# Kernel tuning notes

Measured on AMD Instinct MI355X. Metric: run time of the kernel, lower is better.

The kernel has to match this reference:

```python
import jax, jax.numpy as jnp
import numpy as np

N_OBJS = 100          # max detections / scatter buffer size
TOP_K = 100           # top_k_n peaks per channel
KP_THRES = 0.3        # score threshold before NMS
NMS_IOU = 0.5
RESIZE_H, RESIZE_W = 1536.0, 1536.0   # resize_shape (== heatmap HxW here)
H, W = 1536, 1536


def _peak_hms(hms):
    # 3x3 stride-1 SAME max pool; keep only local maxima (Base.apply_max_pool)
    hmax = jax.lax.reduce_window(hms, -jnp.inf, jax.lax.max, (1, 3, 3, 1), (1, 1, 1, 1), 'SAME')
    return jnp.where(hms == hmax, hms, 0.0)


def _top_k_loc(hms, k):
    # per-channel top-k peak coordinates -> [b, c, k, 2] (y, x) int32
    b, h, w, c = hms.shape
    flat = jnp.transpose(hms, (0, 3, 1, 2)).reshape(b, c, h * w)
    _, idx = jax.lax.top_k(flat, k)
    return jnp.stack([idx // w, idx % w], axis=-1).astype(jnp.int32)


def _iou_matrix(boxes):
    # boxes [N,4] = (y1,x1,y2,x2)
    y1, x1, y2, x2 = boxes[:, 0], boxes[:, 1], boxes[:, 2], boxes[:, 3]
    area = jnp.maximum(y2 - y1, 0.0) * jnp.maximum(x2 - x1, 0.0)
    iy1 = jnp.maximum(y1[:, None], y1[None, :]); ix1 = jnp.maximum(x1[:, None], x1[None, :])
    iy2 = jnp.minimum(y2[:, None], y2[None, :]); ix2 = jnp.minimum(x2[:, None], x2[None, :])
    inter = jnp.maximum(iy2 - iy1, 0.0) * jnp.maximum(ix2 - ix1, 0.0)
    union = area[:, None] + area[None, :] - inter
    return inter / jnp.maximum(union, 1e-8)


def _nms_single(boxes, scores):
    # greedy single-class NMS, fixed-size (combined_non_max_suppression equivalent,
    # clip_boxes=False, score_threshold=-inf); padded slots are zeros like TF.
    order = jnp.argsort(-scores)
    boxes, scores = boxes[order], scores[order]
    n = boxes.shape[0]
    iou = _iou_matrix(boxes)
    idxs = jnp.arange(n)

    def step(suppressed, inp):
        i, iou_row = inp
        keep_i = ~suppressed[i]
        return suppressed | (keep_i & (iou_row > NMS_IOU) & (idxs > i)), keep_i

    _, keep = jax.lax.scan(step, jnp.zeros(n, bool), (idxs, iou))
    perm = jnp.argsort(jnp.where(keep, 0, 1))  # stable: compact kept to front, score order preserved
    keep_s = keep[perm]
    out_boxes = jnp.where(keep_s[:, None], boxes[perm], 0.0)
    out_scores = jnp.where(keep_s, scores[perm], 0.0)
    return out_boxes, out_scores, jnp.zeros(n, jnp.float32)


def _forward(obj_heat_map, offset_map, size_maps, origin_shapes):
    resize_shape = jnp.array([RESIZE_H, RESIZE_W], jnp.float32)
    ratio = origin_shapes / resize_shape                      # [b,2]
    hms = _peak_hms(obj_heat_map)                             # [b,H,W,2]
    b = hms.shape[0]
    coors = _top_k_loc(hms, TOP_K)                            # [b,2,K,2]
    b_coors, b_lnmks = coors[:, :1], coors[:, 1:]             # obj / nose coords
    bidx = jnp.arange(b)[:, None, None]

    # nose landmark: scores at nose-channel peaks, masked mean of coords (int mean like TF)
    nose_scores = hms[bidx, b_lnmks[..., 0], b_lnmks[..., 1], 1]     # [b,1,K]
    nose_mask = nose_scores > 0.5
    cnt = jnp.maximum(jnp.sum(nose_mask), 1)
    lnmk_mean = jnp.sum(jnp.where(nose_mask[..., None], b_lnmks, 0), axis=(0, 1, 2)) // cnt
    b_lnmks_m = lnmk_mean.reshape(b, 1, 2)                    # requires b == 1 (as in original)
    b_nose_scores = jnp.where(nose_mask, nose_scores, -1.0).reshape(b, -1)

    # boxes from sizes at object peaks
    size_vals = size_maps[bidx, b_coors[..., 0], b_coors[..., 1]]    # [b,1,K,2]
    obj_scores = hms[bidx, b_coors[..., 0], b_coors[..., 1], 0]      # [b,1,K]
    centers = b_coors.astype(jnp.float32)
    tls = jnp.maximum(centers - size_vals / 2.0, 0.0)
    brs = jnp.minimum(centers + size_vals / 2.0, resize_shape - 1.0)
    bboxes = jnp.concatenate([tls, brs], axis=-1) * jnp.tile(ratio, (1, 2))[:, None, None, :]
    bboxes, scores = bboxes[:, 0], obj_scores[:, 0]           # [b,K,4], [b,K]

    # scatter masked candidates into -1-initialized buffer (tensor_scatter_nd_update equivalent)
    mask = scores > KP_THRES
    cand = jnp.where(mask[..., None], jnp.concatenate([bboxes, scores[..., None]], -1), -1.0)
    cand = jnp.pad(cand, ((0, 0), (0, N_OBJS - TOP_K), (0, 0)), constant_values=-1.0)  # [b,N_OBJS,5]

    nb, ns, nc = jax.vmap(_nms_single)(cand[..., :4], cand[..., 4])
    box_results = jnp.where(nb == -1.0, jnp.inf, nb)
    box_results = jnp.where(box_results == 0.0, jnp.inf, box_results)  # (x - 1 == -1)
    b_bboxes = jnp.concatenate([box_results, ns[..., None], nc[..., None]], axis=-1)  # [b,N_OBJS,6]

    # offset vectors at the mean nose landmark (gather 8ch -> [b,n,4,2])
    bidx2 = jnp.arange(b)[:, None]
    off = offset_map[bidx2, b_lnmks_m[..., 0], b_lnmks_m[..., 1]].reshape(b, 1, 4, 2)
    lf = b_lnmks_m.astype(jnp.float32)
    b_ENM = (lf[:, :, None, :] - off) * ratio[:, None, None, :]
    b_lnmks_out = lf * ratio[:, None, :]
    return b_bboxes, b_lnmks_out, b_ENM, b_nose_scores


def setup_inputs() -> dict:
    key = jax.random.key(0)
    k1, k2, k3 = jax.random.split(key, 3)
    obj_heat_map = jax.random.uniform(k1, (1, H, W, 2), jnp.float32)
    offset_map = jax.random.normal(k2, (1, H, W, 8), jnp.float32) * 8.0
    size_maps = jax.random.uniform(k3, (1, H, W, 2), jnp.float32) * 128.0
    origin_shapes = jnp.array([[1080.0, 1920.0]], jnp.float32)
    return {"obj_heat_map": obj_heat_map, "offset_map": offset_map,
            "size_maps": size_maps, "origin_shapes": origin_shapes}


def reference(obj_heat_map, offset_map, size_maps, origin_shapes):
    return _forward(obj_heat_map, offset_map, size_maps, origin_shapes)
```

## Files before the change

kernel.cpp:

```cpp
#include <hip/hip_runtime.h>
#include <cstdint>

#define IW 1536
#define IH 1536
#define TOPK 100
#define CAPP 327680
#define CAPB 128
#define CAPM 16384
#define BF_INF16 0x7F7Fu

typedef unsigned u32; typedef unsigned long long u64; typedef unsigned short u16;

#define OH1   0
#define OCNT  512
#define OSEL  516
#define OPK   520
#define OPV   (OPK + 2*CAPP)
#define OMID  (OPV + CAPP)

__device__ __forceinline__ u32 enc16(u32 b){ b &= 0xFFFFu; return (b & 0x8000u) ? ((~b)&0xFFFFu) : (b|0x8000u); }
__device__ __forceinline__ u32 dec16(u32 e){ return (e & 0x8000u) ? (e^0x8000u) : ((~e)&0xFFFFu); }
__device__ __forceinline__ float up16(u32 b){ return __uint_as_float((b&0xFFFFu)<<16); }
__device__ __forceinline__ u16 f2bf(float f){ u32 u=__float_as_uint(f); return (u16)((u + 0x7FFFu + ((u>>16)&1u))>>16); }

__device__ __forceinline__ void wave_sel256(const u32* bins, u32 need, int* Dout, u32* Aout){
  int lane = threadIdx.x & 63;
  u32 s = bins[lane*4] + bins[lane*4+1] + bins[lane*4+2] + bins[lane*4+3];
  u32 c = s;
  #pragma unroll
  for(int off=1;off<64;off<<=1){
    u32 v = __shfl_down(c, off, 64);
    if(lane + off < 64) c += v;
  }
  u32 cnext = __shfl_down(c, 1, 64); if(lane==63) cnext = 0u;
  u64 m = __ballot(c >= need);
  if(m == 0ull){ if(lane==0){ *Dout = 0; *Aout = 0u; } return; }
  int L = 63 - __builtin_clzll(m);
  if(lane == L){
    u32 above = cnext; int D = 4*L;
    for(int b=4*L+3; b>=4*L; --b){
      u32 h = bins[b];
      if(above + h >= need){ D = b; break; }
      above += h;
    }
    *Dout = D; *Aout = above;
  }
}

__global__ __launch_bounds__(1024) void scan_kernel(const u32* __restrict__ hm, u32* __restrict__ ws){
  __shared__ u32 lh[512];
  __shared__ u32 lbuf[2][1600];
  __shared__ u16 vbuf[2][1600];
  __shared__ u32 lcnt[2], lbase[2];
  int tid = threadIdx.x, lane = tid & 63;
  for(int i=tid;i<512;i+=1024) lh[i]=0u;
  if(tid<2) lcnt[tid]=0u;
  __syncthreads();

  int p = (blockIdx.x*1024 + tid)*4;
  int y = p / IW, x = p - y*IW;
  const u32* R1 = hm + y*IW;
  const u32* R0 = y ? R1 - IW : R1;
  const u32* R2 = (y < IH-1) ? R1 + IW : R1;
  uint4 c0 = *(const uint4*)(R0+x), c1 = *(const uint4*)(R1+x), c2 = *(const uint4*)(R2+x);
  int xl = x ? x-1 : 0, xr = (x+4 < IW) ? x+4 : IW-1;
  u32 a0[6] = {R0[xl], c0.x, c0.y, c0.z, c0.w, R0[xr]};
  u32 a1[6] = {R1[xl], c1.x, c1.y, c1.z, c1.w, R1[xr]};
  u32 a2[6] = {R2[xl], c2.x, c2.y, c2.z, c2.w, R2[xr]};

  #pragma unroll
  for(int j=0;j<4;++j){
    u32 cc = a1[j+1];
    u32 cl = cc & 0xFFFFu, chv = cc >> 16;
    u32 m0=0u, m1=0u;
    #pragma unroll
    for(int d=0;d<3;++d){
      u32 n0=a0[j+d], n2=a2[j+d]; u32 t;
      t=n0&0xFFFFu; m0=t>m0?t:m0;  t=n0>>16; m1=t>m1?t:m1;
      t=n2&0xFFFFu; m0=t>m0?t:m0;  t=n2>>16; m1=t>m1?t:m1;
    }
    { u32 n=a1[j];   u32 t=n&0xFFFFu; m0=t>m0?t:m0; t=n>>16; m1=t>m1?t:m1; }
    { u32 n=a1[j+2]; u32 t=n&0xFFFFu; m0=t>m0?t:m0; t=n>>16; m1=t>m1?t:m1; }
    bool pk0 = (cl >= m0), pk1 = (chv >= m1);
    u32 idx = (u32)(p + j);

    u64 mk0 = __ballot(pk0);
    if(mk0){
      u32 cw = __popcll(mk0), b;
      if(lane==0) b = atomicAdd(&lcnt[0], cw);
      b = __shfl(b, 0);
      if(pk0){
        u32 pos = b + __popcll(mk0 & ((1ull<<lane)-1ull));
        if(pos < 1600){ lbuf[0][pos] = idx; vbuf[0][pos] = (u16)cl; }
      }
    }
    u64 mk1 = __ballot(pk1);
    if(mk1){
      u32 cw = __popcll(mk1), b;
      if(lane==0) b = atomicAdd(&lcnt[1], cw);
      b = __shfl(b, 0);
      if(pk1){
        u32 pos = b + __popcll(mk1 & ((1ull<<lane)-1ull));
        if(pos < 1600){ lbuf[1][pos] = idx; vbuf[1][pos] = (u16)chv; }
      }
    }
    if(pk0) atomicAdd(&lh[enc16(cl)>>8], 1u);
    if(pk1) atomicAdd(&lh[256 + (enc16(chv)>>8)], 1u);
  }
  __syncthreads();
  if(tid < 2){
    u32 n = lcnt[tid]; if(n > 1600) n = 1600;
    lcnt[tid] = n;
    lbase[tid] = atomicAdd(&ws[OCNT+tid], n);
  }
  __syncthreads();
  u16* pv = (u16*)(ws + OPV);
  for(int ch=0;ch<2;++ch){
    u32 n = lcnt[ch], base = lbase[ch];
    for(u32 i=tid;i<n;i+=1024){
      u32 g = base + i;
      if(g < CAPP){ ws[OPK + ch*CAPP + g] = lbuf[ch][i]; pv[ch*CAPP + g] = vbuf[ch][i]; }
    }
  }
  for(int i=tid;i<512;i+=1024) if(lh[i]) atomicAdd(&ws[OH1+i], lh[i]);
}

#define GRID2 128
__global__ __launch_bounds__(1024) void mid_kernel(u32* __restrict__ ws){
  __shared__ u32 lhh[512];
  __shared__ u64 mbuf[2][2048];
  __shared__ u32 mcnt[2], mbase[2];
  __shared__ int Dsh[2]; __shared__ u32 Ash[2];
  int tid = threadIdx.x, lane = tid & 63;
  if(tid < 512) lhh[tid] = ws[OH1+tid];
  if(tid < 2) mcnt[tid] = 0u;
  __syncthreads();
  if(tid < 64){
    wave_sel256(lhh,       (u32)TOPK, &Dsh[0], &Ash[0]);
    wave_sel256(lhh + 256, (u32)TOPK, &Dsh[1], &Ash[1]);
  }
  __syncthreads();
  if(blockIdx.x == 0 && tid < 2){ ws[OSEL+tid] = (u32)Dsh[tid]; ws[OSEL+2+tid] = Ash[tid]; }

  const u16* pv = (const u16*)(ws + OPV);
  for(int ch=0;ch<2;++ch){
    u32 n = ws[OCNT+ch]; if(n > CAPP) n = CAPP;
    int D = Dsh[ch];
    for(u32 base = blockIdx.x*1024; base < n; base += GRID2*1024){
      u32 i = base + tid;
      bool act = (i < n);
      u32 e = 0, idx = 0;
      if(act){ e = enc16(pv[ch*CAPP + i]); idx = ws[OPK + ch*CAPP + i]; }
      bool hit = act && ((int)(e>>8) >= D);
      u64 mk = __ballot(hit);
      if(mk){
        u32 cw = __popcll(mk), b;
        if(lane==0) b = atomicAdd(&mcnt[ch], cw);
        b = __shfl(b, 0);
        if(hit){
          u32 pos = b + __popcll(mk & ((1ull<<lane)-1ull));
          if(pos < 2048) mbuf[ch][pos] = ((u64)e<<32) | (u32)(~idx);
        }
      }
    }
  }
  __syncthreads();
  if(tid < 2){
    u32 c = mcnt[tid]; if(c > 2048) c = 2048;
    mcnt[tid] = c;
    mbase[tid] = atomicAdd(&ws[OCNT+2+tid], c);
  }
  __syncthreads();
  u64* mid = (u64*)(ws + OMID);
  for(int ch=0;ch<2;++ch)
    for(u32 i=tid;i<mcnt[ch];i+=1024){
      u32 g = mbase[ch] + i;
      if(g < CAPM) mid[ch*CAPM + g] = mbuf[ch][i];
    }
}

__global__ __launch_bounds__(1024) void finalize_kernel(
    u32* __restrict__ ws, const u32* __restrict__ szm, const u16* __restrict__ offm,
    const u16* __restrict__ orig, u16* __restrict__ out){
  __shared__ u64 keys[CAPB];
  __shared__ u32 lsd[256];
  __shared__ u32 h2[2048];
  __shared__ u32 wbits[64];
  __shared__ u32 sel[CAPB];
  __shared__ int Bv, selc, selc2, Lsh; __shared__ u32 Aul;
  __shared__ float oval[TOPK]; __shared__ int oidx[TOPK];
  __shared__ float nval[TOPK]; __shared__ int nidx[TOPK];
  __shared__ float cbox[TOPK][4]; __shared__ float cscore[TOPK]; __shared__ float area[TOPK];
  __shared__ int sup[TOPK]; __shared__ int slotv[TOPK];
  __shared__ u64 nbits[2*TOPK];
  __shared__ u64 suppS[2];
  __shared__ int cS, srS, scS, meanr, meanc;
  int tid = threadIdx.x, lane = tid & 63;

  if(tid < TOPK){ oval[tid]=0.0f; oidx[tid]=0; nval[tid]=0.0f; nidx[tid]=0; }
  __syncthreads();

  for(int ch=0; ch<2; ++ch){
    int nM = (int)ws[OCNT+2+ch]; if(nM > CAPM) nM = CAPM;
    int D = (int)ws[OSEL+ch];
    u32 above = ws[OSEL+2+ch];
    const u64* mid = ((const u64*)(ws + OMID)) + ch*CAPM;
    float* dval = ch ? nval : oval;
    int*   didx = ch ? nidx : oidx;

    for(int i=tid;i<2048;i+=1024) h2[i]=0u;
    if(tid < 256) lsd[tid]=0u;
    if(tid < 64) wbits[tid]=0u;
    if(tid == 0){ selc = 0; selc2 = 0; Bv = 0; }
    __syncthreads();

    for(int i=tid;i<nM;i+=1024){
      u64 k = mid[i]; u32 e = (u32)(k>>32);
      if((int)(e>>8) == D) atomicAdd(&lsd[e&255], 1u);
      else { int pos = atomicAdd(&selc, 1); if(pos < CAPB) keys[pos] = k; }
    }
    __syncthreads();
    u32 need2 = (u32)TOPK - above;
    if(tid < 64) wave_sel256(lsd, need2, &Lsh, &Aul);
    __syncthreads();
    u32 thr = ((u32)D<<8) | (u32)Lsh;
    float tval = up16(dec16(thr));

    for(int i=tid;i<nM;i+=1024){
      u64 k = mid[i]; u32 e = (u32)(k>>32);
      if(e > thr && (e>>8) == (u32)D){
        int pos = atomicAdd(&selc, 1); if(pos < CAPB) keys[pos] = k;
      } else if(e == thr){
        u32 idx = ~(u32)(k & 0xFFFFFFFFu);
        atomicAdd(&h2[idx>>11], 1u);
      }
    }
    __syncthreads();
    int nA = selc; if(nA > CAPB) nA = CAPB; if(nA > TOPK) nA = TOPK;
    if(tid < nA){
      u64 kreg = keys[tid];
      int r = 0;
      for(int j=0;j<nA;++j) r += (keys[j] > kreg);
      if(r < TOPK){
        dval[r] = up16(dec16((u32)(kreg>>32)));
        didx[r] = (int)(~(u32)(kreg & 0xFFFFFFFFu));
      }
    }
    int need = TOPK - nA;

    if(need > 0){
      if(tid < 64){
        int base = tid*32;
        u32 s = 0;
        #pragma unroll
        for(int k2=0;k2<32;++k2) s += h2[base+k2];
        u32 c = s;
        #pragma unroll
        for(int off=1;off<64;off<<=1){
          u32 v = __shfl_up(c, off, 64);
          if(lane >= off) c += v;
        }
        u64 m = __ballot(c >= (u32)need);
        int L = (int)(__ffsll((unsigned long long)m) - 1);
        if(tid == L){
          u32 cum2 = c - s;
          int B = base;
          for(int k2=0;k2<32;++k2){
            u32 hb = h2[base+k2];
            if(cum2 + hb >= (u32)need){ B = base+k2; break; }
            cum2 += hb;
          }
          Bv = B;
        }
      }
      __syncthreads();
      int B = Bv;
      for(int i=tid;i<nM;i+=1024){
        u64 k = mid[i]; u32 e = (u32)(k>>32);
        if(e == thr){
          u32 idx = ~(u32)(k & 0xFFFFFFFFu);
          int b = (int)(idx>>11);
          if(b < B){
            int pos = atomicAdd(&selc2, 1);
            if(pos < CAPB) sel[pos] = idx;
          } else if(b == B){
            atomicOr(&wbits[(idx&2047)>>5], 1u<<(idx&31));
          }
        }
      }
      __syncthreads();
      int sc = selc2; if(sc > CAPB) sc = CAPB;
      if(tid < sc){
        u32 v = sel[tid];
        int r = 0;
        for(int j=0;j<sc;++j) r += (sel[j] < v);
        if(nA + r < TOPK){ dval[nA+r] = tval; didx[nA+r] = (int)v; }
      }
      if(tid == 0){
        int rem = need - sc;
        int pos = nA + sc;
        for(int wi=0; wi<64 && rem>0; ++wi){
          u32 bits = wbits[wi];
          while(bits && rem>0){
            int l = __ffs(bits) - 1;
            bits &= bits - 1;
            if(pos < TOPK){ dval[pos] = tval; didx[pos] = (int)(((u32)B<<11) | ((u32)wi<<5) | (u32)l); }
            ++pos; --rem;
          }
        }
      }
    }
    __syncthreads();
  }

  float ry = up16(orig[0]) / 1536.0f;
  float rx = up16(orig[1]) / 1536.0f;

  if(tid == 0){ cS = 0; srS = 0; scS = 0; }
  __syncthreads();
  if(tid < TOPK && nval[tid] > 0.5f){
    atomicAdd(&cS, 1);
    atomicAdd(&srS, nidx[tid] / IW);
    atomicAdd(&scS, nidx[tid] % IW);
  }
  if(tid < TOPK) out[610 + tid] = f2bf(nval[tid] > 0.5f ? nval[tid] : -1.0f);
  __syncthreads();
  if(tid == 0){
    int c = cS < 1 ? 1 : cS;
    meanr = srS / c; meanc = scS / c;
  }

  if(tid < TOPK){
    int idx = oidx[tid];
    int r = idx / IW, c = idx - r*IW;
    float score = oval[tid];
    u32 sz = szm[idx];
    float sy = up16(sz), sx = up16(sz>>16);
    float cy = (float)r, cx = (float)c;
    float tly = fmaxf(cy - sy*0.5f, 0.0f);
    float tlx = fmaxf(cx - sx*0.5f, 0.0f);
    float bry = fminf(cy + sy*0.5f, 1535.0f);
    float brx = fminf(cx + sx*0.5f, 1535.0f);
    bool mk = score > 0.3f;
    float b0 = mk ? tly*ry : -1.0f;
    float b1 = mk ? tlx*rx : -1.0f;
    float b2 = mk ? bry*ry : -1.0f;
    float b3 = mk ? brx*rx : -1.0f;
    cbox[tid][0]=b0; cbox[tid][1]=b1; cbox[tid][2]=b2; cbox[tid][3]=b3;
    cscore[tid] = mk ? score : -1.0f;
    area[tid] = fmaxf(b2-b0,0.0f) * fmaxf(b3-b1,0.0f);
  }
  if(tid < 2*TOPK) nbits[tid] = 0ull;
  __syncthreads();

  for(int t=tid; t<TOPK*TOPK; t+=1024){
    int i = t / TOPK, j = t - i*TOPK;
    if(j > i){
      float iy1 = fmaxf(cbox[i][0], cbox[j][0]);
      float ix1 = fmaxf(cbox[i][1], cbox[j][1]);
      float iy2 = fminf(cbox[i][2], cbox[j][2]);
      float ix2 = fminf(cbox[i][3], cbox[j][3]);
      float inter = fmaxf(iy2-iy1,0.0f) * fmaxf(ix2-ix1,0.0f);
      float uni = (area[i] + area[j]) - inter;
      if(inter / fmaxf(uni, 1e-8f) > 0.5f)
        atomicOr(&nbits[i*2 + (j>>6)], 1ull << (j&63));
    }
  }
  __syncthreads();
  if(tid == 0){
    u64 s0 = 0ull, s1 = 0ull;
    for(int i=0;i<TOPK;++i){
      bool su = (i<64) ? ((s0>>i)&1ull) : ((s1>>(i-64))&1ull);
      if(!su){ s0 |= nbits[i*2]; s1 |= nbits[i*2+1]; }
    }
    suppS[0] = s0; suppS[1] = s1;
  }
  __syncthreads();
  if(tid < TOPK) sup[tid] = (int)((suppS[tid>>6] >> (tid&63)) & 1ull);
  __syncthreads();

  if(tid < TOPK){
    int kbefore = 0, sbefore = 0, ktot = 0;
    for(int j=0;j<TOPK;++j){
      int sj = sup[j];
      ktot += (1 - sj);
      if(j < tid){ kbefore += (1 - sj); sbefore += sj; }
    }
    int slot = sup[tid] ? (ktot + sbefore) : kbefore;
    slotv[slot] = tid;
  }
  __syncthreads();

  if(tid < TOPK){
    int s = slotv[tid];
    bool ks = !sup[s];
    u16 row[6];
    if(ks){
      for(int d=0;d<4;++d){
        float v = cbox[s][d];
        row[d] = (v == -1.0f || v == 0.0f) ? (u16)BF_INF16 : f2bf(v);
      }
      row[4] = f2bf(cscore[s]);
    } else {
      for(int d=0;d<4;++d) row[d] = (u16)BF_INF16;
      row[4] = 0;
    }
    row[5] = 0;
    for(int d=0;d<6;++d) out[tid*6 + d] = row[d];
  }

  if(tid == 0){
    float lfy = (float)meanr, lfx = (float)meanc;
    out[600] = f2bf(lfy * ry);
    out[601] = f2bf(lfx * rx);
    const u16* op = offm + ((size_t)meanr*IW + meanc)*8;
    for(int p=0;p<4;++p){
      out[602 + p*2 + 0] = f2bf((lfy - up16(op[p*2+0])) * ry);
      out[602 + p*2 + 1] = f2bf((lfx - up16(op[p*2+1])) * rx);
    }
  }
}

extern "C" void kernel_launch(void* const* d_in, const int* in_sizes, int n_in,
                              void* d_out, int out_size, void* d_ws, size_t ws_size,
                              hipStream_t stream) {
  const u32* heat = (const u32*)d_in[0];
  const u16* offm = (const u16*)d_in[1];
  const u32* szm  = (const u32*)d_in[2];
  const u16* orig = (const u16*)d_in[3];
  u16* out = (u16*)d_out;
  u32* ws = (u32*)d_ws;

  hipMemsetAsync(ws, 0, 520*sizeof(u32), stream);
  scan_kernel<<<576, 1024, 0, stream>>>(heat, ws);
  mid_kernel<<<GRID2, 1024, 0, stream>>>(ws);
  finalize_kernel<<<1, 1024, 0, stream>>>(ws, szm, offm, orig, out);
}
```

Baseline: 187.0 us.

## Refine first-pass radix histogram to 11 bits and aggregate second-level bin atomics

The first-level histogram of peak scores now uses 2048 bins per channel (11 bits of the bf16 key) instead of 256. The coarse threshold therefore lands much closer to the final top-k boundary, and fewer candidates reach the single-block finalize kernel. The finalize kernel's 32-bin second pass uses wave-ballot aggregation to cut shared-memory atomic contention. The cost is more global and shared histogram traffic and a larger memset in the scan and mid kernels. CAPM is also raised as headroom for the candidate buffer.

```diff
diff --git a/kernel.cpp b/kernel.cpp
--- a/kernel.cpp
+++ b/kernel.cpp
@@ -6,15 +6,15 @@
 #define TOPK 100
 #define CAPP 327680
 #define CAPB 128
-#define CAPM 16384
+#define CAPM 32768
 #define BF_INF16 0x7F7Fu
 
 typedef unsigned u32; typedef unsigned long long u64; typedef unsigned short u16;
 
 #define OH1   0
-#define OCNT  512
-#define OSEL  516
-#define OPK   520
+#define OCNT  4096
+#define OSEL  4100
+#define OPK   4104
 #define OPV   (OPK + 2*CAPP)
 #define OMID  (OPV + CAPP)
 
@@ -23,9 +23,11 @@
 __device__ __forceinline__ float up16(u32 b){ return __uint_as_float((b&0xFFFFu)<<16); }
 __device__ __forceinline__ u16 f2bf(float f){ u32 u=__float_as_uint(f); return (u16)((u + 0x7FFFu + ((u>>16)&1u))>>16); }
 
-__device__ __forceinline__ void wave_sel256(const u32* bins, u32 need, int* Dout, u32* Aout){
+__device__ __forceinline__ void wave_sel2048(const u32* bins, u32 need, int* Dout, u32* Aout){
   int lane = threadIdx.x & 63;
-  u32 s = bins[lane*4] + bins[lane*4+1] + bins[lane*4+2] + bins[lane*4+3];
+  u32 s = 0;
+  #pragma unroll
+  for(int k=0;k<32;++k) s += bins[lane*32+k];
   u32 c = s;
   #pragma unroll
   for(int off=1;off<64;off<<=1){
@@ -35,10 +37,10 @@
   u32 cnext = __shfl_down(c, 1, 64); if(lane==63) cnext = 0u;
   u64 m = __ballot(c >= need);
   if(m == 0ull){ if(lane==0){ *Dout = 0; *Aout = 0u; } return; }
-  int L = 63 - __builtin_clzll(m);
+  int L = 63 - __builtin_clzll((unsigned long long)m);
   if(lane == L){
-    u32 above = cnext; int D = 4*L;
-    for(int b=4*L+3; b>=4*L; --b){
+    u32 above = cnext; int D = 32*L;
+    for(int b=32*L+31; b>=32*L; --b){
       u32 h = bins[b];
       if(above + h >= need){ D = b; break; }
       above += h;
@@ -48,12 +50,12 @@
 }
 
 __global__ __launch_bounds__(1024) void scan_kernel(const u32* __restrict__ hm, u32* __restrict__ ws){
-  __shared__ u32 lh[512];
+  __shared__ u32 lh[4096];
   __shared__ u32 lbuf[2][1600];
   __shared__ u16 vbuf[2][1600];
   __shared__ u32 lcnt[2], lbase[2];
   int tid = threadIdx.x, lane = tid & 63;
-  for(int i=tid;i<512;i+=1024) lh[i]=0u;
+  for(int i=tid;i<4096;i+=1024) lh[i]=0u;
   if(tid<2) lcnt[tid]=0u;
   __syncthreads();
 
@@ -104,8 +106,8 @@
         if(pos < 1600){ lbuf[1][pos] = idx; vbuf[1][pos] = (u16)chv; }
       }
     }
-    if(pk0) atomicAdd(&lh[enc16(cl)>>8], 1u);
-    if(pk1) atomicAdd(&lh[256 + (enc16(chv)>>8)], 1u);
+    if(pk0) atomicAdd(&lh[enc16(cl)>>5], 1u);
+    if(pk1) atomicAdd(&lh[2048 + (enc16(chv)>>5)], 1u);
   }
   __syncthreads();
   if(tid < 2){
@@ -122,23 +124,21 @@
       if(g < CAPP){ ws[OPK + ch*CAPP + g] = lbuf[ch][i]; pv[ch*CAPP + g] = vbuf[ch][i]; }
     }
   }
-  for(int i=tid;i<512;i+=1024) if(lh[i]) atomicAdd(&ws[OH1+i], lh[i]);
+  for(int i=tid;i<4096;i+=1024) if(lh[i]) atomicAdd(&ws[OH1+i], lh[i]);
 }
 
 #define GRID2 128
 __global__ __launch_bounds__(1024) void mid_kernel(u32* __restrict__ ws){
-  __shared__ u32 lhh[512];
+  __shared__ u32 lhh[4096];
   __shared__ u64 mbuf[2][2048];
   __shared__ u32 mcnt[2], mbase[2];
   __shared__ int Dsh[2]; __shared__ u32 Ash[2];
   int tid = threadIdx.x, lane = tid & 63;
-  if(tid < 512) lhh[tid] = ws[OH1+tid];
+  for(int i=tid;i<4096;i+=1024) lhh[i] = ws[OH1+i];
   if(tid < 2) mcnt[tid] = 0u;
   __syncthreads();
-  if(tid < 64){
-    wave_sel256(lhh,       (u32)TOPK, &Dsh[0], &Ash[0]);
-    wave_sel256(lhh + 256, (u32)TOPK, &Dsh[1], &Ash[1]);
-  }
+  if(tid < 64)                wave_sel2048(lhh,        (u32)TOPK, &Dsh[0], &Ash[0]);
+  else if(tid < 128)          wave_sel2048(lhh + 2048, (u32)TOPK, &Dsh[1], &Ash[1]);
   __syncthreads();
   if(blockIdx.x == 0 && tid < 2){ ws[OSEL+tid] = (u32)Dsh[tid]; ws[OSEL+2+tid] = Ash[tid]; }
 
@@ -151,7 +151,7 @@
       bool act = (i < n);
       u32 e = 0, idx = 0;
       if(act){ e = enc16(pv[ch*CAPP + i]); idx = ws[OPK + ch*CAPP + i]; }
-      bool hit = act && ((int)(e>>8) >= D);
+      bool hit = act && ((int)(e>>5) >= D);
       u64 mk = __ballot(hit);
       if(mk){
         u32 cw = __popcll(mk), b;
@@ -183,11 +183,11 @@
     u32* __restrict__ ws, const u32* __restrict__ szm, const u16* __restrict__ offm,
     const u16* __restrict__ orig, u16* __restrict__ out){
   __shared__ u64 keys[CAPB];
-  __shared__ u32 lsd[256];
+  __shared__ u32 lsd[32];
   __shared__ u32 h2[2048];
   __shared__ u32 wbits[64];
   __shared__ u32 sel[CAPB];
-  __shared__ int Bv, selc, selc2, Lsh; __shared__ u32 Aul;
+  __shared__ int Bv, selc, selc2, Lsh;
   __shared__ float oval[TOPK]; __shared__ int oidx[TOPK];
   __shared__ float nval[TOPK]; __shared__ int nidx[TOPK];
   __shared__ float cbox[TOPK][4]; __shared__ float cscore[TOPK]; __shared__ float area[TOPK];
@@ -209,30 +209,56 @@
     int*   didx = ch ? nidx : oidx;
 
     for(int i=tid;i<2048;i+=1024) h2[i]=0u;
-    if(tid < 256) lsd[tid]=0u;
+    if(tid < 32) lsd[tid]=0u;
     if(tid < 64) wbits[tid]=0u;
     if(tid == 0){ selc = 0; selc2 = 0; Bv = 0; }
     __syncthreads();
 
-    for(int i=tid;i<nM;i+=1024){
-      u64 k = mid[i]; u32 e = (u32)(k>>32);
-      if((int)(e>>8) == D) atomicAdd(&lsd[e&255], 1u);
-      else { int pos = atomicAdd(&selc, 1); if(pos < CAPB) keys[pos] = k; }
+    for(int base=0; base<nM; base+=1024){
+      int i = base + tid;
+      u64 k = 0; u32 e = 0;
+      bool inb = (i < nM);
+      if(inb){ k = mid[i]; e = (u32)(k>>32); }
+      bool hi = inb && ((int)(e>>5) > D);
+      if(hi){ int pos = atomicAdd(&selc, 1); if(pos < CAPB) keys[pos] = k; }
+      bool isD = inb && ((int)(e>>5) == D);
+      u32 bin = e & 31u;
+      u64 pend = __ballot(isD);
+      while(pend){
+        int leader = (int)(__ffsll((unsigned long long)pend) - 1);
+        u32 lb = __shfl(bin, leader);
+        u64 same = __ballot(isD && bin == lb);
+        if(lane == leader) atomicAdd(&lsd[lb], (u32)__popcll(same));
+        pend &= ~same;
+      }
     }
     __syncthreads();
     u32 need2 = (u32)TOPK - above;
-    if(tid < 64) wave_sel256(lsd, need2, &Lsh, &Aul);
+    if(tid < 64){
+      u32 v = (lane < 32) ? lsd[lane] : 0u;
+      u32 c = v;
+      #pragma unroll
+      for(int off=1;off<32;off<<=1){
+        u32 t = __shfl_down(c, off, 64);
+        if(lane + off < 32) c += t;
+      }
+      u64 m = __ballot((lane < 32) && c >= need2);
+      if(lane == 0) Lsh = m ? (63 - __builtin_clzll((unsigned long long)m)) : 0;
+    }
     __syncthreads();
-    u32 thr = ((u32)D<<8) | (u32)Lsh;
+    u32 thr = ((u32)D<<5) | (u32)Lsh;
     float tval = up16(dec16(thr));
 
-    for(int i=tid;i<nM;i+=1024){
-      u64 k = mid[i]; u32 e = (u32)(k>>32);
-      if(e > thr && (e>>8) == (u32)D){
-        int pos = atomicAdd(&selc, 1); if(pos < CAPB) keys[pos] = k;
-      } else if(e == thr){
-        u32 idx = ~(u32)(k & 0xFFFFFFFFu);
-        atomicAdd(&h2[idx>>11], 1u);
+    for(int base=0; base<nM; base+=1024){
+      int i = base + tid;
+      if(i < nM){
+        u64 k = mid[i]; u32 e = (u32)(k>>32);
+        if(e > thr && (e>>5) == (u32)D){
+          int pos = atomicAdd(&selc, 1); if(pos < CAPB) keys[pos] = k;
+        } else if(e == thr){
+          u32 idx = ~(u32)(k & 0xFFFFFFFFu);
+          atomicAdd(&h2[idx>>11], 1u);
+        }
       }
     }
     __syncthreads();
@@ -275,16 +301,19 @@
       }
       __syncthreads();
       int B = Bv;
-      for(int i=tid;i<nM;i+=1024){
-        u64 k = mid[i]; u32 e = (u32)(k>>32);
-        if(e == thr){
-          u32 idx = ~(u32)(k & 0xFFFFFFFFu);
-          int b = (int)(idx>>11);
-          if(b < B){
-            int pos = atomicAdd(&selc2, 1);
-            if(pos < CAPB) sel[pos] = idx;
-          } else if(b == B){
-            atomicOr(&wbits[(idx&2047)>>5], 1u<<(idx&31));
+      for(int base=0; base<nM; base+=1024){
+        int i = base + tid;
+        if(i < nM){
+          u64 k = mid[i]; u32 e = (u32)(k>>32);
+          if(e == thr){
+            u32 idx = ~(u32)(k & 0xFFFFFFFFu);
+            int b = (int)(idx>>11);
+            if(b < B){
+              int pos = atomicAdd(&selc2, 1);
+              if(pos < CAPB) sel[pos] = idx;
+            } else if(b == B){
+              atomicOr(&wbits[(idx&2047)>>5], 1u<<(idx&31));
+            }
           }
         }
       }
@@ -304,7 +333,7 @@
           while(bits && rem>0){
             int l = __ffs(bits) - 1;
             bits &= bits - 1;
-            if(pos < TOPK){ dval[pos] = tval; didx[pos] = (int)(((u32)B<<11) | ((u32)wi<<5) | (u32)l); }
+            if(pos < TOPK){ dval[pos] = tval; didx[pos] = (int)(((u32)Bv<<11) | ((u32)wi<<5) | (u32)l); }
             ++pos; --rem;
           }
         }
@@ -431,7 +460,7 @@
   u16* out = (u16*)d_out;
   u32* ws = (u32*)d_ws;
 
-  hipMemsetAsync(ws, 0, 520*sizeof(u32), stream);
+  hipMemsetAsync(ws, 0, 4104*sizeof(u32), stream);
   scan_kernel<<<576, 1024, 0, stream>>>(heat, ws);
   mid_kernel<<<GRID2, 1024, 0, stream>>>(ws);
   finalize_kernel<<<1, 1024, 0, stream>>>(ws, szm, offm, orig, out);
```

Result: slower. 290.4 us (+55.3%).
